# Performance work log

Hardware: AMD Instinct MI355X
Metric: run time of the kernel (lower is better)

Reference implementation:

```python
import jax, jax.numpy as jnp
import numpy as np

N, E, NNZ, R, F = 100000, 100000, 800000, 4, 64

def setup_inputs() -> dict:
    key = jax.random.key(0)
    k1, k2, k3, k4, k5 = jax.random.split(key, 5)
    x = jax.random.normal(k1, (N, F), dtype=jnp.float32)
    rank_masks = jax.random.uniform(k2, (R, E), dtype=jnp.float32)
    vals = jnp.ones((NNZ,), dtype=jnp.float32)
    he_idxs = jax.random.randint(k3, (E,), 0, E, dtype=jnp.int64)
    rows = jax.random.randint(k4, (NNZ,), 0, N, dtype=jnp.int64)
    cols = jax.random.randint(k5, (NNZ,), 0, E, dtype=jnp.int64)
    return {"x": x, "rank_masks": rank_masks, "vals": vals,
            "he_idxs": he_idxs, "rows": rows, "cols": cols}

def reference(x, rank_masks, vals, he_idxs, rows, cols):
    # incidence: sparse [N, E] in COO form (rows=node idx, cols=hyperedge idx, vals)
    n, f = x.shape
    r = rank_masks.shape[0]
    e = he_idxs.shape[0]
    # hyperedge_features = incidence^T @ x  -> [E, F]  (gather nodes, scatter to hyperedges)
    he_feat = jax.ops.segment_sum(x[rows] * vals[:, None], cols, num_segments=e)
    # rank_masks[:, he_idxs] -> [R, E]; einsum('ij,jk->jik') -> [E, R, F]
    rm = rank_masks[:, he_idxs]
    ranks_features = rm.T[:, :, None] * he_feat[:, None, :]          # [E, R, F]
    flat = ranks_features.reshape(e, r * f)                          # [E, R*F]
    # sequences = incidence @ flat -> [N, R*F]
    seq = jax.ops.segment_sum(flat[cols] * vals[:, None], rows, num_segments=n)
    seq = seq.reshape(n, r, f)
    # last rank slot is the node's own features
    seq = seq.at[:, -1, :].set(x)
    return seq
```

## Files before the change

### kernel.cpp

```cpp
#include <hip/hip_runtime.h>

static constexpr int F   = 64;
static constexpr int RF  = 256;
static constexpr int CAP = 48;


__global__ void k_wv(const int* __restrict__ he_idxs, const float* __restrict__ rm,
                     float4* __restrict__ wv, int E)
{
    int e = blockIdx.x * 256 + threadIdx.x;
    if (e >= E) return;
    int idx = he_idxs[e];
    float4 w;
    w.x = rm[idx];
    w.y = rm[(size_t)E + idx];
    w.z = rm[2 * (size_t)E + idx];
    w.w = 0.f;
    wv[e] = w;
}

__global__ void k_scatter_col(const int* __restrict__ rows, const int* __restrict__ cols,
                              const float* __restrict__ vals,
                              int* __restrict__ cur_col, int2* __restrict__ col_pay,
                              int nnz, int E)
{
    int t = blockIdx.x * 256 + threadIdx.x;
    if (t >= nnz) return;
    int c = cols[t];
    int j = atomicAdd(&cur_col[c], 1);
    if (j < CAP)
        col_pay[(size_t)j * E + c] = make_int2(rows[t], __float_as_int(vals[t]));
}

__global__ void k_scatter_row(const int* __restrict__ rows, const int* __restrict__ cols,
                              const float* __restrict__ vals,
                              int* __restrict__ cur_row, int2* __restrict__ row_pay,
                              int nnz, int Nn)
{
    int t = blockIdx.x * 256 + threadIdx.x;
    if (t >= nnz) return;
    int r = rows[t];
    int j = atomicAdd(&cur_row[r], 1);
    if (j < CAP)
        row_pay[(size_t)j * Nn + r] = make_int2(__float_as_int(vals[t]), cols[t]);
}

__device__ inline float4 group_reduce4(float4 a)
{
    a.x += __shfl_xor(a.x, 16); a.y += __shfl_xor(a.y, 16);
    a.z += __shfl_xor(a.z, 16); a.w += __shfl_xor(a.w, 16);
    a.x += __shfl_xor(a.x, 32); a.y += __shfl_xor(a.y, 32);
    a.z += __shfl_xor(a.z, 32); a.w += __shfl_xor(a.w, 32);
    return a;
}

__global__ void k_hefeat_fixed(const float* __restrict__ x,
                               const int* __restrict__ cur_col,
                               const int2* __restrict__ col_pay,
                               float* __restrict__ he, int E)
{
    int wave = threadIdx.x >> 6, lane = threadIdx.x & 63;
    int g = lane >> 4, li = lane & 15;
    int e = blockIdx.x * 4 + wave;
    if (e >= E) return;
    int cnt = min(cur_col[e], CAP);
    float4 acc = make_float4(0.f, 0.f, 0.f, 0.f);
    for (int j = g; j < cnt; j += 4) {
        int2 cp = col_pay[(size_t)j * E + e];
        float v = __int_as_float(cp.y);
        float4 xv = ((const float4*)(x + (size_t)cp.x * F))[li];
        acc.x += v * xv.x; acc.y += v * xv.y;
        acc.z += v * xv.z; acc.w += v * xv.w;
    }
    acc = group_reduce4(acc);
    if (g == 0)
        ((float4*)(he + (size_t)e * F))[li] = acc;
}

__global__ void k_seq_fixed(const int* __restrict__ cur_row,
                            const int2* __restrict__ row_pay,
                            const float4* __restrict__ wv,
                            const float* __restrict__ he,
                            const float* __restrict__ x,
                            float* __restrict__ out, int Nn)
{
    int wave = threadIdx.x >> 6, lane = threadIdx.x & 63;
    int g = lane >> 4, li = lane & 15;
    int n = blockIdx.x * 4 + wave;
    if (n >= Nn) return;
    int cnt = min(cur_row[n], CAP);
    float4 a0 = make_float4(0.f, 0.f, 0.f, 0.f);
    float4 a1 = a0, a2 = a0;
    for (int j = g; j < cnt; j += 4) {
        int2 rp = row_pay[(size_t)j * Nn + n];
        float v = __int_as_float(rp.x);
        int e = rp.y;
        float4 w = wv[e];
        float4 h = ((const float4*)(he + (size_t)e * F))[li];
        float s0 = w.x * v, s1 = w.y * v, s2 = w.z * v;
        a0.x += s0 * h.x; a0.y += s0 * h.y; a0.z += s0 * h.z; a0.w += s0 * h.w;
        a1.x += s1 * h.x; a1.y += s1 * h.y; a1.z += s1 * h.z; a1.w += s1 * h.w;
        a2.x += s2 * h.x; a2.y += s2 * h.y; a2.z += s2 * h.z; a2.w += s2 * h.w;
    }
    a0 = group_reduce4(a0);
    a1 = group_reduce4(a1);
    a2 = group_reduce4(a2);
    if (g == 0) {
        float4* o = (float4*)(out + (size_t)n * RF);
        o[li]      = a0;
        o[16 + li] = a1;
        o[32 + li] = a2;
        o[48 + li] = ((const float4*)(x + (size_t)n * F))[li];
    }
}

__global__ void k_hefeat_atomic(const float* __restrict__ x,
                                const float* __restrict__ vals,
                                const int* __restrict__ rows,
                                const int* __restrict__ cols,
                                float* __restrict__ out, int nnz)
{
    int t = blockIdx.x * 256 + threadIdx.x;
    int k = t >> 6;
    if (k >= nnz) return;
    int f = t & 63;
    atomicAdd(out + (size_t)cols[k] * RF + 3 * F + f,
              x[(size_t)rows[k] * F + f] * vals[k]);
}

__global__ void k_seq_atomic(const float* __restrict__ rank_masks,
                             const float* __restrict__ vals,
                             const int* __restrict__ he_idxs,
                             const int* __restrict__ rows,
                             const int* __restrict__ cols,
                             float* __restrict__ out, int nnz, int E)
{
    int t = blockIdx.x * 256 + threadIdx.x;
    int k = t >> 6;
    if (k >= nnz) return;
    int f = t & 63;
    int n = rows[k], e = cols[k];
    float v = vals[k];
    int idx = he_idxs[e];
    float hf = out[(size_t)e * RF + 3 * F + f] * v;
    float* base = out + (size_t)n * RF + f;
    atomicAdd(base + 0 * F, rank_masks[idx] * hf);
    atomicAdd(base + 1 * F, rank_masks[(size_t)E + idx] * hf);
    atomicAdd(base + 2 * F, rank_masks[2 * (size_t)E + idx] * hf);
}

__global__ void k_lastrank(const float* __restrict__ x,
                           float* __restrict__ out, int n_nodes)
{
    int t = blockIdx.x * 256 + threadIdx.x;
    if (t >= n_nodes * 16) return;
    int n = t >> 4, li = t & 15;
    ((float4*)(out + (size_t)n * RF + 3 * F))[li] =
        ((const float4*)(x + (size_t)n * F))[li];
}


extern "C" void kernel_launch(void* const* d_in, const int* in_sizes, int n_in,
                              void* d_out, int out_size, void* d_ws, size_t ws_size,
                              hipStream_t stream)
{
    const float* x       = (const float*)d_in[0];
    const float* rm      = (const float*)d_in[1];
    const float* vals    = (const float*)d_in[2];
    const int*   he_idxs = (const int*)d_in[3];
    const int*   rows    = (const int*)d_in[4];
    const int*   cols    = (const int*)d_in[5];
    float* out = (float*)d_out;

    const int nnz = in_sizes[2];
    const int E   = in_sizes[3];
    const int nN  = in_sizes[0] / F;

    const int nnz_blocks  = (nnz + 255) / 256;
    const int seg_blocks  = (E + 3) / 4;
    const int node_blocks = (nN + 3) / 4;
    const int e_blocks    = (E + 255) / 256;

    {
        char* p = (char*)d_ws;
        float* he      = (float*)p;  p += (size_t)E * F * sizeof(float);
        int2*  row_pay = (int2*)p;   p += (size_t)CAP * nN * sizeof(int2);
        int2*  col_pay = (int2*)p;   p += (size_t)CAP * E * sizeof(int2);
        float4* wv     = (float4*)p; p += (size_t)E * sizeof(float4);
        int*   cur_row = (int*)p;    p += (size_t)nN * sizeof(int);
        int*   cur_col = (int*)p;    p += (size_t)E * sizeof(int);
        size_t need_fixed = (size_t)(p - (char*)d_ws);

        if (ws_size >= need_fixed) {
            hipMemsetAsync(cur_row, 0, ((size_t)nN + E) * sizeof(int), stream);
            k_wv<<<e_blocks, 256, 0, stream>>>(he_idxs, rm, wv, E);
            k_scatter_col<<<nnz_blocks, 256, 0, stream>>>(rows, cols, vals,
                                                          cur_col, col_pay, nnz, E);
            k_scatter_row<<<nnz_blocks, 256, 0, stream>>>(rows, cols, vals,
                                                          cur_row, row_pay, nnz, nN);
            k_hefeat_fixed<<<seg_blocks, 256, 0, stream>>>(x, cur_col, col_pay, he, E);
            k_seq_fixed<<<node_blocks, 256, 0, stream>>>(cur_row, row_pay, wv, he,
                                                         x, out, nN);
            return;
        }
    }

    hipMemsetAsync(d_out, 0, (size_t)out_size * sizeof(float), stream);
    const int b64 = (nnz * 64 + 255) / 256;
    const int lr_blocks = (nN * 16 + 255) / 256;
    k_hefeat_atomic<<<b64, 256, 0, stream>>>(x, vals, rows, cols, out, nnz);
    k_seq_atomic<<<b64, 256, 0, stream>>>(rm, vals, he_idxs, rows, cols, out, nnz, E);
    k_lastrank<<<lr_blocks, 256, 0, stream>>>(x, out, nN);
}
```

Baseline: 206.1 us.

## Store gathered node and hyperedge features in bf16 and fuse prep/scatter kernels

Converts x to a bf16 copy in a prep kernel that also builds the rank-weight table, and stores hyperedge features in bf16. This halves the bytes of the random gathers in both segment-sum kernels. The separate row and column scatter kernels are merged into one to cut a launch and reread of the COO arrays. The cost is an extra pass over x to convert it, plus bf16 rounding of intermediates that may exceed tolerance.

```diff
diff --git a/kernel.cpp b/kernel.cpp
--- a/kernel.cpp
+++ b/kernel.cpp
@@ -4,45 +4,64 @@
 static constexpr int RF  = 256;
 static constexpr int CAP = 48;
 
-
-__global__ void k_wv(const int* __restrict__ he_idxs, const float* __restrict__ rm,
-                     float4* __restrict__ wv, int E)
-{
-    int e = blockIdx.x * 256 + threadIdx.x;
-    if (e >= E) return;
-    int idx = he_idxs[e];
-    float4 w;
-    w.x = rm[idx];
-    w.y = rm[(size_t)E + idx];
-    w.z = rm[2 * (size_t)E + idx];
-    w.w = 0.f;
-    wv[e] = w;
-}
-
-__global__ void k_scatter_col(const int* __restrict__ rows, const int* __restrict__ cols,
-                              const float* __restrict__ vals,
-                              int* __restrict__ cur_col, int2* __restrict__ col_pay,
-                              int nnz, int E)
+__device__ inline float bf2f(unsigned int u16) {
+    return __uint_as_float(u16 << 16);
+}
+__device__ inline unsigned short f2bf(float f) {
+    unsigned int x = __float_as_uint(f);
+    return (unsigned short)((x + 0x7fffu + ((x >> 16) & 1u)) >> 16);
+}
+__device__ inline float4 bf4_to_f4(uint2 u) {
+    float4 r;
+    r.x = bf2f(u.x & 0xffffu);
+    r.y = bf2f(u.x >> 16);
+    r.z = bf2f(u.y & 0xffffu);
+    r.w = bf2f(u.y >> 16);
+    return r;
+}
+__device__ inline uint2 f4_to_bf4(float4 f) {
+    uint2 u;
+    u.x = (unsigned int)f2bf(f.x) | ((unsigned int)f2bf(f.y) << 16);
+    u.y = (unsigned int)f2bf(f.z) | ((unsigned int)f2bf(f.w) << 16);
+    return u;
+}
+
+
+__global__ void k_prep(const int* __restrict__ he_idxs, const float* __restrict__ rm,
+                       const float* __restrict__ x,
+                       float4* __restrict__ wv, uint2* __restrict__ x_bf,
+                       int E, int Nn)
+{
+    int t = blockIdx.x * 256 + threadIdx.x;
+    if (t < E) {
+        int idx = he_idxs[t];
+        float4 w;
+        w.x = rm[idx];
+        w.y = rm[(size_t)E + idx];
+        w.z = rm[2 * (size_t)E + idx];
+        w.w = 0.f;
+        wv[t] = w;
+    }
+    if (t < Nn * 16) {
+        float4 v = ((const float4*)x)[t];
+        x_bf[t] = f4_to_bf4(v);
+    }
+}
+
+__global__ void k_scatter(const int* __restrict__ rows, const int* __restrict__ cols,
+                          const float* __restrict__ vals,
+                          int* __restrict__ cur_row, int* __restrict__ cur_col,
+                          int2* __restrict__ row_pay, int2* __restrict__ col_pay,
+                          int nnz, int E, int Nn)
 {
     int t = blockIdx.x * 256 + threadIdx.x;
     if (t >= nnz) return;
-    int c = cols[t];
-    int j = atomicAdd(&cur_col[c], 1);
-    if (j < CAP)
-        col_pay[(size_t)j * E + c] = make_int2(rows[t], __float_as_int(vals[t]));
-}
-
-__global__ void k_scatter_row(const int* __restrict__ rows, const int* __restrict__ cols,
-                              const float* __restrict__ vals,
-                              int* __restrict__ cur_row, int2* __restrict__ row_pay,
-                              int nnz, int Nn)
-{
-    int t = blockIdx.x * 256 + threadIdx.x;
-    if (t >= nnz) return;
-    int r = rows[t];
-    int j = atomicAdd(&cur_row[r], 1);
-    if (j < CAP)
-        row_pay[(size_t)j * Nn + r] = make_int2(__float_as_int(vals[t]), cols[t]);
+    int r = rows[t], c = cols[t];
+    int vb = __float_as_int(vals[t]);
+    int jc = atomicAdd(&cur_col[c], 1);
+    if (jc < CAP) col_pay[(size_t)jc * E + c] = make_int2(r, vb);
+    int jr = atomicAdd(&cur_row[r], 1);
+    if (jr < CAP) row_pay[(size_t)jr * Nn + r] = make_int2(vb, c);
 }
 
 __device__ inline float4 group_reduce4(float4 a)
@@ -54,10 +73,10 @@
     return a;
 }
 
-__global__ void k_hefeat_fixed(const float* __restrict__ x,
-                               const int* __restrict__ cur_col,
-                               const int2* __restrict__ col_pay,
-                               float* __restrict__ he, int E)
+__global__ void k_hefeat(const uint2* __restrict__ x_bf,
+                         const int* __restrict__ cur_col,
+                         const int2* __restrict__ col_pay,
+                         uint2* __restrict__ he_bf, int E)
 {
     int wave = threadIdx.x >> 6, lane = threadIdx.x & 63;
     int g = lane >> 4, li = lane & 15;
@@ -68,21 +87,21 @@
     for (int j = g; j < cnt; j += 4) {
         int2 cp = col_pay[(size_t)j * E + e];
         float v = __int_as_float(cp.y);
-        float4 xv = ((const float4*)(x + (size_t)cp.x * F))[li];
+        float4 xv = bf4_to_f4(x_bf[(size_t)cp.x * 16 + li]);
         acc.x += v * xv.x; acc.y += v * xv.y;
         acc.z += v * xv.z; acc.w += v * xv.w;
     }
     acc = group_reduce4(acc);
     if (g == 0)
-        ((float4*)(he + (size_t)e * F))[li] = acc;
-}
-
-__global__ void k_seq_fixed(const int* __restrict__ cur_row,
-                            const int2* __restrict__ row_pay,
-                            const float4* __restrict__ wv,
-                            const float* __restrict__ he,
-                            const float* __restrict__ x,
-                            float* __restrict__ out, int Nn)
+        he_bf[(size_t)e * 16 + li] = f4_to_bf4(acc);
+}
+
+__global__ void k_seq(const int* __restrict__ cur_row,
+                      const int2* __restrict__ row_pay,
+                      const float4* __restrict__ wv,
+                      const uint2* __restrict__ he_bf,
+                      const float* __restrict__ x,
+                      float* __restrict__ out, int Nn)
 {
     int wave = threadIdx.x >> 6, lane = threadIdx.x & 63;
     int g = lane >> 4, li = lane & 15;
@@ -96,7 +115,7 @@
         float v = __int_as_float(rp.x);
         int e = rp.y;
         float4 w = wv[e];
-        float4 h = ((const float4*)(he + (size_t)e * F))[li];
+        float4 h = bf4_to_f4(he_bf[(size_t)e * 16 + li]);
         float s0 = w.x * v, s1 = w.y * v, s2 = w.z * v;
         a0.x += s0 * h.x; a0.y += s0 * h.y; a0.z += s0 * h.z; a0.w += s0 * h.w;
         a1.x += s1 * h.x; a1.y += s1 * h.y; a1.z += s1 * h.z; a1.w += s1 * h.w;
@@ -179,11 +198,12 @@
     const int nnz_blocks  = (nnz + 255) / 256;
     const int seg_blocks  = (E + 3) / 4;
     const int node_blocks = (nN + 3) / 4;
-    const int e_blocks    = (E + 255) / 256;
+    const int prep_blocks = ((nN * 16 > E ? nN * 16 : E) + 255) / 256;
 
     {
         char* p = (char*)d_ws;
-        float* he      = (float*)p;  p += (size_t)E * F * sizeof(float);
+        uint2* he_bf   = (uint2*)p;  p += (size_t)E * 16 * sizeof(uint2);
+        uint2* x_bf    = (uint2*)p;  p += (size_t)nN * 16 * sizeof(uint2);
         int2*  row_pay = (int2*)p;   p += (size_t)CAP * nN * sizeof(int2);
         int2*  col_pay = (int2*)p;   p += (size_t)CAP * E * sizeof(int2);
         float4* wv     = (float4*)p; p += (size_t)E * sizeof(float4);
@@ -193,14 +213,13 @@
 
         if (ws_size >= need_fixed) {
             hipMemsetAsync(cur_row, 0, ((size_t)nN + E) * sizeof(int), stream);
-            k_wv<<<e_blocks, 256, 0, stream>>>(he_idxs, rm, wv, E);
-            k_scatter_col<<<nnz_blocks, 256, 0, stream>>>(rows, cols, vals,
-                                                          cur_col, col_pay, nnz, E);
-            k_scatter_row<<<nnz_blocks, 256, 0, stream>>>(rows, cols, vals,
-                                                          cur_row, row_pay, nnz, nN);
-            k_hefeat_fixed<<<seg_blocks, 256, 0, stream>>>(x, cur_col, col_pay, he, E);
-            k_seq_fixed<<<node_blocks, 256, 0, stream>>>(cur_row, row_pay, wv, he,
-                                                         x, out, nN);
+            k_prep<<<prep_blocks, 256, 0, stream>>>(he_idxs, rm, x, wv, x_bf, E, nN);
+            k_scatter<<<nnz_blocks, 256, 0, stream>>>(rows, cols, vals,
+                                                      cur_row, cur_col,
+                                                      row_pay, col_pay, nnz, E, nN);
+            k_hefeat<<<seg_blocks, 256, 0, stream>>>(x_bf, cur_col, col_pay, he_bf, E);
+            k_seq<<<node_blocks, 256, 0, stream>>>(cur_row, row_pay, wv, he_bf,
+                                                   x, out, nN);
             return;
         }
     }
```

Result: slower. 238.4 us (+15.7%).
